# Kernel optimization log

Hardware: AMD Instinct MI355X
Metric: run time of the kernel (lower is better)

The kernel has to match this reference:

```python
import jax, jax.numpy as jnp
import numpy as np

B, H0, W0, C, NH, A, P = 32, 56, 56, 256, 8, 49, 7  # P = pool_size = sqrt(agent_num)
KS = 3  # depthwise conv kernel


def setup_inputs() -> dict:
    key = jax.random.key(0)
    ks = jax.random.split(key, 12)
    f32 = jnp.float32
    inp = {
        "x": jax.random.normal(ks[0], (B, H0 * W0, C), f32),
        "qkv_w": jax.random.normal(ks[1], (C, 3 * C), f32) * 0.02,   # used as x @ qkv_w
        "qkv_b": jax.random.normal(ks[2], (3 * C,), f32) * 0.02,
        "proj_w": jax.random.normal(ks[3], (C, C), f32) * 0.02,
        "proj_b": jax.random.normal(ks[4], (C,), f32) * 0.02,
        "dwc_w": jax.random.normal(ks[5], (C, 1, KS, KS), f32) * 0.1,  # depthwise OIHW, groups=C
        "dwc_b": jnp.zeros((C,), f32),
        "an_bias": jax.random.normal(ks[6], (NH, A, 7, 7), f32) * 0.02,
        "na_bias": jax.random.normal(ks[7], (NH, A, 7, 7), f32) * 0.02,
        "ah_bias": jax.random.normal(ks[8], (1, NH, A, H0, 1), f32) * 0.02,
        "aw_bias": jax.random.normal(ks[9], (1, NH, A, 1, W0), f32) * 0.02,
        "ha_bias": jax.random.normal(ks[10], (1, NH, H0, 1, A), f32) * 0.02,
        "wa_bias": jax.random.normal(ks[11], (1, NH, 1, W0, A), f32) * 0.02,
        "h": H0,
        "w": W0,
    }
    return inp


def _resize(t, hw):
    # bilinear (half-pixel, align_corners=False) resize of the last two dims
    return jax.image.resize(t, t.shape[:-2] + tuple(hw), method="bilinear")


def reference(x, qkv_w, qkv_b, proj_w, proj_b, dwc_w, dwc_b,
              an_bias, na_bias, ah_bias, aw_bias, ha_bias, wa_bias, h, w):
    b, n, c = x.shape
    nh = an_bias.shape[0]
    hd = c // nh
    a = an_bias.shape[1]
    p = int(a ** 0.5)
    scale = hd ** -0.5

    qkv = x @ qkv_w + qkv_b                      # (b, n, 3c)
    q, k, v = jnp.split(qkv, 3, axis=-1)

    # agent tokens: adaptive avg pool of q over (h, w) -> (p, p); exact since h%p==0
    q_img = q.reshape(b, h, w, c)
    agent = q_img.reshape(b, p, h // p, p, w // p, c).mean(axis=(2, 4)).reshape(b, a, c)

    q = q.reshape(b, n, nh, hd).transpose(0, 2, 1, 3)       # (b, nh, n, hd)
    k = k.reshape(b, n, nh, hd).transpose(0, 2, 1, 3)
    v = v.reshape(b, n, nh, hd).transpose(0, 2, 1, 3)
    agent = agent.reshape(b, a, nh, hd).transpose(0, 2, 1, 3)  # (b, nh, a, hd)

    def agent2token_bias(bias):  # (nh, a, h0, w0) -> (1, nh, a, n)
        pb = _resize(bias, (h, w)).reshape(nh, p, p, h * w).transpose(0, 3, 1, 2)
        pb = _resize(pb, (p, p)).reshape(nh, h * w, a).transpose(0, 2, 1)
        return pb[None]

    def token2agent_bias(bias):  # (nh, a, h0, w0) -> (1, nh, n, a)
        ab = _resize(bias, (h, w)).reshape(nh, p, p, h * w).transpose(0, 3, 1, 2)
        ab = _resize(ab, (p, p)).reshape(nh, h * w, a)
        return ab[None]

    position_bias = agent2token_bias(an_bias) + agent2token_bias((ah_bias + aw_bias)[0])
    agent_bias = token2agent_bias(na_bias) + \
        token2agent_bias((ha_bias + wa_bias)[0].transpose(0, 3, 1, 2))

    # stage 1: agent tokens attend to keys/values
    agent_attn = jax.nn.softmax(
        jnp.einsum('bhad,bhnd->bhan', agent * scale, k) + position_bias, axis=-1)
    agent_v = jnp.einsum('bhan,bhnd->bhad', agent_attn, v)      # (b, nh, a, hd)

    # stage 2: queries attend to agent tokens
    q_attn = jax.nn.softmax(
        jnp.einsum('bhnd,bhad->bhna', q * scale, agent) + agent_bias, axis=-1)
    out = jnp.einsum('bhna,bhad->bhnd', q_attn, agent_v)        # (b, nh, n, hd)
    out = out.transpose(0, 2, 1, 3).reshape(b, n, c)

    # depthwise conv on v
    v_img = v.transpose(0, 2, 1, 3).reshape(b, h, w, c).transpose(0, 3, 1, 2)  # NCHW
    dwc = jax.lax.conv_general_dilated(
        v_img, dwc_w, window_strides=(1, 1), padding='SAME',
        feature_group_count=c, dimension_numbers=('NCHW', 'OIHW', 'NCHW'))
    dwc = dwc + dwc_b[None, :, None, None]
    out = out + dwc.transpose(0, 2, 3, 1).reshape(b, n, c)

    return out @ proj_w + proj_b
```

## Files before the change

kernel.cpp:

```cpp
#include <hip/hip_runtime.h>
#include <stdint.h>

#define B_ 32
#define H_ 56
#define W_ 56
#define N_ 3136
#define C_ 256
#define NH_ 8
#define HD_ 32
#define A_ 49
#define NCH_ 7
#define CHK_ 448
#define SCALE_ 0.17677669529663687f

typedef _Float16 h16;
typedef __attribute__((ext_vector_type(4))) _Float16 h16x4;
typedef __attribute__((ext_vector_type(8))) _Float16 h16x8;
typedef __attribute__((ext_vector_type(4))) float f32x4;

__device__ __forceinline__ void gload16(const void* g, void* l) {
  __builtin_amdgcn_global_load_lds(
      (const __attribute__((address_space(1))) unsigned int*)(uintptr_t)g,
      (__attribute__((address_space(3))) unsigned int*)(unsigned int)(uintptr_t)l,
      16, 0, 0);
}

__global__ __launch_bounds__(256)
void bias_kernel(const float* __restrict__ an, const float* __restrict__ na,
                 const float* __restrict__ ah, const float* __restrict__ aw,
                 const float* __restrict__ ha, const float* __restrict__ wa,
                 float* __restrict__ posb, float* __restrict__ agbt)
{
  const int hh = blockIdx.x / A_;
  const int ag = blockIdx.x % A_;
  __shared__ float an7[A_], na7[A_], ahv[H_], awv[W_], hav[H_], wav[W_];
  const int tid = threadIdx.x;
  if (tid < A_) {
    an7[tid] = an[(hh*A_ + ag)*A_ + tid];
    na7[tid] = na[(hh*A_ + ag)*A_ + tid];
  }
  if (tid < H_) {
    ahv[tid] = ah[(hh*A_ + ag)*H_ + tid];
    awv[tid] = aw[(hh*A_ + ag)*W_ + tid];
    hav[tid] = ha[(hh*H_ + tid)*A_ + ag];
    wav[tid] = wa[(hh*W_ + tid)*A_ + ag];
  }
  __syncthreads();
  for (int t = tid; t < N_; t += 256) {
    const int ty = t / W_, tx = t % W_;
    const float py = (ty + 0.5f)*0.125f - 0.5f;
    const float px = (tx + 0.5f)*0.125f - 0.5f;
    const int iy = (int)floorf(py), ix = (int)floorf(px);
    const float fy = py - (float)iy, fx = px - (float)ix;
    const int iy0 = min(max(iy, 0), 6), iy1 = min(iy + 1, 6);
    const int ix0 = min(max(ix, 0), 6), ix1 = min(ix + 1, 6);
    const float w00 = (1.f-fy)*(1.f-fx), w01 = (1.f-fy)*fx;
    const float w10 = fy*(1.f-fx),       w11 = fy*fx;
    const float ban = w00*an7[iy0*7+ix0] + w01*an7[iy0*7+ix1]
                    + w10*an7[iy1*7+ix0] + w11*an7[iy1*7+ix1];
    const float bna = w00*na7[iy0*7+ix0] + w01*na7[iy0*7+ix1]
                    + w10*na7[iy1*7+ix0] + w11*na7[iy1*7+ix1];
    posb[((size_t)(hh*A_ + ag))*N_ + t] = ban + ahv[ty] + awv[tx];
    agbt[((size_t)(hh*A_ + ag))*N_ + t] = bna + hav[ty] + wav[tx];
  }
}

__global__ __launch_bounds__(256)
void convx_kernel(const float* __restrict__ x, h16* __restrict__ xh)
{
  const size_t nchunk = (size_t)B_*N_*C_/8;
  const size_t stride = (size_t)gridDim.x * 256;
  for (size_t i = blockIdx.x*256 + threadIdx.x; i < nchunk; i += stride) {
    const float4 u = ((const float4*)x)[i*2];
    const float4 v = ((const float4*)x)[i*2+1];
    h16x8 o;
    o[0]=(h16)u.x; o[1]=(h16)u.y; o[2]=(h16)u.z; o[3]=(h16)u.w;
    o[4]=(h16)v.x; o[5]=(h16)v.y; o[6]=(h16)v.z; o[7]=(h16)v.w;
    ((h16x8*)xh)[i] = o;
  }
}

__global__ __launch_bounds__(256)
void convw_kernel(const float* __restrict__ qkvw, const float* __restrict__ projw,
                  const float* __restrict__ dwcw, const float* __restrict__ dwcb,
                  h16* __restrict__ wtq, h16* __restrict__ wtp, h16* __restrict__ w9t)
{
  const int bid = blockIdx.x, k = threadIdx.x;
  if (bid < 768) {
    wtq[bid*256 + k] = (h16)qkvw[(size_t)k*768 + bid];
  } else if (bid < 1024) {
    const int n = bid - 768;
    wtp[n*256 + k] = (h16)projw[(size_t)k*256 + n];
  } else {
    const int row = bid - 1024;
    w9t[row*256 + k] = (h16)(row < 9 ? dwcw[k*9 + row] : dwcb[k]);
  }
}

__device__ __forceinline__ void gemm_tile_128(
    const h16* __restrict__ Ag, const h16* __restrict__ Bg,
    int m0, int n0, char* lds, f32x4 acc[4][4], int lane, int wr, int wc, int tid)
{
  int aoff[4], boff[4];
  #pragma unroll
  for (int r = 0; r < 4; ++r) {
    const int row = wr*64 + r*16 + (lane & 15);
    const int ps  = (lane >> 4) ^ ((row >> 1) & 3);
    aoff[r] = row*64 + ps*16;
  }
  #pragma unroll
  for (int c = 0; c < 4; ++c) {
    const int nrow = wc*64 + c*16 + (lane & 15);
    const int ps   = (lane >> 4) ^ ((nrow >> 1) & 3);
    boff[c] = 8192 + nrow*64 + ps*16;
  }
  const int i0 = tid, i1 = tid + 256;
  const int r0 = i0 >> 2, s0 = (i0 & 3) ^ ((r0 >> 1) & 3);
  const int r1 = i1 >> 2, s1 = (i1 & 3) ^ ((r1 >> 1) & 3);

  for (int k0 = 0; k0 < 256; k0 += 32) {
    __syncthreads();
    gload16(Ag + (size_t)(m0 + r0)*256 + k0 + s0*8, lds + i0*16);
    gload16(Ag + (size_t)(m0 + r1)*256 + k0 + s1*8, lds + i1*16);
    gload16(Bg + (size_t)(n0 + r0)*256 + k0 + s0*8, lds + 8192 + i0*16);
    gload16(Bg + (size_t)(n0 + r1)*256 + k0 + s1*8, lds + 8192 + i1*16);
    __syncthreads();
    h16x8 af[4], bf[4];
    #pragma unroll
    for (int r = 0; r < 4; ++r) af[r] = *(const h16x8*)(lds + aoff[r]);
    #pragma unroll
    for (int c = 0; c < 4; ++c) bf[c] = *(const h16x8*)(lds + boff[c]);
    #pragma unroll
    for (int r = 0; r < 4; ++r)
      #pragma unroll
      for (int c = 0; c < 4; ++c)
        acc[r][c] = __builtin_amdgcn_mfma_f32_16x16x32_f16(af[r], bf[c], acc[r][c], 0, 0, 0);
  }
}

__global__ __launch_bounds__(256)
void gemm_qkv_mfma(const h16* __restrict__ xh, const h16* __restrict__ wtq,
                   const float* __restrict__ qkvb,
                   h16* __restrict__ q, h16* __restrict__ k, h16* __restrict__ v)
{
  __shared__ __align__(16) char lds[16384];
  const int tid = threadIdx.x, lane = tid & 63, wid = tid >> 6;
  const int wr = wid & 1, wc = wid >> 1;
  const int m0 = blockIdx.y * 128, n0 = blockIdx.x * 128;
  f32x4 acc[4][4] = {};
  gemm_tile_128(xh, wtq, m0, n0, lds, acc, lane, wr, wc, tid);
  #pragma unroll
  for (int r = 0; r < 4; ++r) {
    #pragma unroll
    for (int reg = 0; reg < 4; ++reg) {
      const int m = m0 + wr*64 + r*16 + (lane >> 4)*4 + reg;
      const int bb = m / N_, t = m % N_;
      #pragma unroll
      for (int c = 0; c < 4; ++c) {
        const int n = n0 + wc*64 + c*16 + (lane & 15);
        const float val = acc[r][c][reg] + qkvb[n];
        const int part = n >> 8, cc = n & 255, hh = cc >> 5, d = cc & 31;
        h16* dst = (part == 0) ? q : ((part == 1) ? k : v);
        dst[(((size_t)(bb*NH_ + hh))*N_ + t)*HD_ + d] = (h16)val;
      }
    }
  }
}

__global__ __launch_bounds__(256)
void gemm_proj_mfma(const h16* __restrict__ preh, const h16* __restrict__ wtp,
                    const float* __restrict__ projb, float* __restrict__ out)
{
  __shared__ __align__(16) char lds[16384];
  const int tid = threadIdx.x, lane = tid & 63, wid = tid >> 6;
  const int wr = wid & 1, wc = wid >> 1;
  const int m0 = blockIdx.y * 128, n0 = blockIdx.x * 128;
  f32x4 acc[4][4] = {};
  gemm_tile_128(preh, wtp, m0, n0, lds, acc, lane, wr, wc, tid);
  #pragma unroll
  for (int r = 0; r < 4; ++r) {
    #pragma unroll
    for (int reg = 0; reg < 4; ++reg) {
      const int m = m0 + wr*64 + r*16 + (lane >> 4)*4 + reg;
      #pragma unroll
      for (int c = 0; c < 4; ++c) {
        const int n = n0 + wc*64 + c*16 + (lane & 15);
        out[(size_t)m*256 + n] = acc[r][c][reg] + projb[n];
      }
    }
  }
}

__global__ __launch_bounds__(64)
void pool_kernel(const h16* __restrict__ q, float* __restrict__ agent)
{
  const int blk = blockIdx.x;
  const int ag = blk % A_;
  const int rem = blk / A_;
  const int tid = threadIdx.x;
  const int d = tid & 31, half = tid >> 5;
  const int ay = ag / 7, ax = ag % 7;
  const size_t base = (size_t)rem * N_ * HD_;
  float s = 0.f;
  #pragma unroll
  for (int it = 0; it < 32; ++it) {
    const int yy = half*4 + (it >> 3), xx = it & 7;
    const int t = (ay*8 + yy)*W_ + ax*8 + xx;
    s += (float)q[base + (size_t)t*HD_ + d];
  }
  s += __shfl_down(s, 32, 64);
  if (tid < 32) agent[(size_t)rem*A_*HD_ + ag*HD_ + d] = s * (1.f/64.f);
}

__global__ __launch_bounds__(256)
void stage1a_mfma(const h16* __restrict__ kmat, const h16* __restrict__ vmat,
                  const float* __restrict__ agent, const float* __restrict__ posb,
                  float* __restrict__ pm, float* __restrict__ pl, float* __restrict__ pacc)
{
  __shared__ __align__(16) h16 Kl[64*32];
  __shared__ __align__(16) h16 Vt[32*72];
  __shared__ __align__(16) h16 Sl[64*72];
  const int tid = threadIdx.x, lane = tid & 63, wid = tid >> 6;
  const int bx = blockIdx.x;
  const int ch = bx % NCH_;
  const int rem = bx / NCH_;
  const int hh = rem & 7;
  const size_t kvbase = (size_t)rem * N_ * HD_;
  const size_t agbase = (size_t)rem * A_ * HD_;
  const float* pb = posb + (size_t)hh*A_*N_;

  const int arow = wid*16 + (lane & 15);
  const int kc = (lane >> 4) * 8;
  h16x8 a_ag = {};
  if (arow < A_) {
    #pragma unroll
    for (int j = 0; j < 8; ++j)
      a_ag[j] = (h16)(agent[agbase + (size_t)arow*HD_ + kc + j] * SCALE_);
  }

  const int r_k = tid >> 2;
  const int s_k = (tid & 3) ^ ((r_k >> 1) & 3);
  const int rowm = (lane >> 4) * 4;
  const int agrow0 = wid*16 + rowm;

  float m_r[4], l_r[4];
  #pragma unroll
  for (int r = 0; r < 4; ++r) { m_r[r] = -1e30f; l_r[r] = 0.f; }
  f32x4 accv[2] = {};

  for (int it = 0; it < 7; ++it) {
    const int t0 = ch*CHK_ + it*64;
    __syncthreads();
    gload16(kmat + kvbase + (size_t)(t0 + r_k)*HD_ + s_k*8, ((char*)Kl) + tid*16);
    const h16x8 vv = *(const h16x8*)&vmat[kvbase + (size_t)(t0 + lane)*HD_ + wid*8];
    #pragma unroll
    for (int j = 0; j < 8; ++j) Vt[(wid*8 + j)*72 + lane] = vv[j];
    __syncthreads();

    float sv[4][4];
    #pragma unroll
    for (int c = 0; c < 4; ++c) {
      const int kr = c*16 + (lane & 15);
      const int ph = (lane >> 4) ^ ((kr >> 1) & 3);
      const h16x8 bf = *(const h16x8*)&Kl[kr*32 + ph*8];
      const f32x4 sc = __builtin_amdgcn_mfma_f32_16x16x32_f16(a_ag, bf, (f32x4){0.f,0.f,0.f,0.f}, 0, 0, 0);
      #pragma unroll
      for (int reg = 0; reg < 4; ++reg) sv[reg][c] = sc[reg];
    }
    #pragma unroll
    for (int reg = 0; reg < 4; ++reg) {
      const int ag = agrow0 + reg;
      if (ag < A_) {
        #pragma unroll
        for (int c = 0; c < 4; ++c)
          sv[reg][c] += pb[(size_t)ag*N_ + t0 + c*16 + (lane & 15)];
      } else {
        #pragma unroll
        for (int c = 0; c < 4; ++c) sv[reg][c] = -1e30f;
      }
      float rm = fmaxf(fmaxf(sv[reg][0], sv[reg][1]), fmaxf(sv[reg][2], sv[reg][3]));
      rm = fmaxf(rm, __shfl_xor(rm, 1));
      rm = fmaxf(rm, __shfl_xor(rm, 2));
      rm = fmaxf(rm, __shfl_xor(rm, 4));
      rm = fmaxf(rm, __shfl_xor(rm, 8));
      const float mn = fmaxf(m_r[reg], rm);
      const float f = __expf(m_r[reg] - mn);
      m_r[reg] = mn;
      float rs = 0.f;
      #pragma unroll
      for (int c = 0; c < 4; ++c) {
        const float p = __expf(sv[reg][c] - mn);
        sv[reg][c] = p;
        rs += p;
      }
      rs += __shfl_xor(rs, 1); rs += __shfl_xor(rs, 2);
      rs += __shfl_xor(rs, 4); rs += __shfl_xor(rs, 8);
      l_r[reg] = l_r[reg]*f + rs;
      accv[0][reg] *= f;
      accv[1][reg] *= f;
      const int row = agrow0 + reg;
      #pragma unroll
      for (int c = 0; c < 4; ++c)
        Sl[row*72 + c*16 + (lane & 15)] = (h16)sv[reg][c];
    }
    __syncthreads();
    const int srow = wid*16 + (lane & 15);
    #pragma unroll
    for (int ks = 0; ks < 2; ++ks) {
      const h16x8 pf = *(const h16x8*)&Sl[srow*72 + ks*32 + (lane >> 4)*8];
      #pragma unroll
      for (int c2 = 0; c2 < 2; ++c2) {
        const int d = c2*16 + (lane & 15);
        const h16x8 vf = *(const h16x8*)&Vt[d*72 + ks*32 + (lane >> 4)*8];
        accv[c2] = __builtin_amdgcn_mfma_f32_16x16x32_f16(pf, vf, accv[c2], 0, 0, 0);
      }
    }
  }

  #pragma unroll
  for (int reg = 0; reg < 4; ++reg) {
    const int ag = agrow0 + reg;
    if (ag < A_) {
      if ((lane & 15) == 0) {
        pm[bx*A_ + ag] = m_r[reg];
        pl[bx*A_ + ag] = l_r[reg];
      }
      #pragma unroll
      for (int c2 = 0; c2 < 2; ++c2)
        pacc[(size_t)bx*(A_*HD_) + (size_t)ag*HD_ + c2*16 + (lane & 15)] = accv[c2][reg];
    }
  }
}

__global__ __launch_bounds__(256)
void stage1b_kernel(const float* __restrict__ pm, const float* __restrict__ pl,
                    const float* __restrict__ pacc, float* __restrict__ agv)
{
  const int rem = blockIdx.x;
  __shared__ float fs[NCH_*A_];
  const int tid = threadIdx.x;
  if (tid < A_) {
    float m = -1e30f;
    #pragma unroll
    for (int ch = 0; ch < NCH_; ++ch) m = fmaxf(m, pm[(rem*NCH_+ch)*A_ + tid]);
    float e[NCH_], l = 0.f;
    #pragma unroll
    for (int ch = 0; ch < NCH_; ++ch) {
      e[ch] = __expf(pm[(rem*NCH_+ch)*A_ + tid] - m);
      l += e[ch] * pl[(rem*NCH_+ch)*A_ + tid];
    }
    const float inv = 1.f / l;
    #pragma unroll
    for (int ch = 0; ch < NCH_; ++ch) fs[ch*A_ + tid] = e[ch] * inv;
  }
  __syncthreads();
  for (int idx = tid; idx < A_*HD_; idx += 256) {
    const int ag = idx >> 5;
    float s = 0.f;
    #pragma unroll
    for (int ch = 0; ch < NCH_; ++ch)
      s += fs[ch*A_ + ag] * pacc[((size_t)(rem*NCH_+ch))*(A_*HD_) + idx];
    agv[(size_t)rem*(A_*HD_) + idx] = s;
  }
}

__global__ __launch_bounds__(256)
void stage2_mfma(const h16* __restrict__ qmat, const float* __restrict__ agent,
                 const float* __restrict__ agv, const float* __restrict__ agbt,
                 h16* __restrict__ preh)
{
  __shared__ __align__(16) char lds2[45568];
  h16* Asw = (h16*)lds2;
  h16* AVt = (h16*)(lds2 + 4096);
  const int tid = threadIdx.x, lane = tid & 63, wid = tid >> 6;
  const int b = blockIdx.y >> 3, hh = blockIdx.y & 7;
  const size_t agbase = (size_t)(b*NH_ + hh)*A_*HD_;

  for (int i = tid; i < 64*32; i += 256) Asw[i] = (h16)0.f;
  for (int i = tid; i < 32*72; i += 256) AVt[i] = (h16)0.f;
  __syncthreads();
  for (int i = tid; i < A_*HD_; i += 256) {
    const int a = i >> 5, d = i & 31;
    Asw[a*32 + (((d >> 3) ^ ((a >> 1) & 3)))*8 + (d & 7)] = (h16)(agent[agbase + i] * SCALE_);
    AVt[d*72 + a] = (h16)agv[agbase + i];
  }
  __syncthreads();

  const int t0 = blockIdx.x*256 + wid*64;
  if (t0 >= N_) return;

  h16* Pl = (h16*)(lds2 + 8704 + wid*9216);
  const h16* qbase = qmat + (size_t)(b*NH_ + hh)*N_*HD_;
  const float* agbt_h = agbt + (size_t)hh*A_*N_;
  const int l15 = lane & 15, g = lane >> 4;

  h16x8 bq[4];
  #pragma unroll
  for (int c = 0; c < 4; ++c) {
    const int a = c*16 + l15;
    const int ph = g ^ ((a >> 1) & 3);
    bq[c] = *(const h16x8*)&Asw[a*32 + ph*8];
  }
  h16x8 aq[4];
  #pragma unroll
  for (int rt = 0; rt < 4; ++rt)
    aq[rt] = *(const h16x8*)&qbase[(size_t)(t0 + rt*16 + l15)*HD_ + g*8];

  f32x4 sc[4][4];
  #pragma unroll
  for (int rt = 0; rt < 4; ++rt)
    #pragma unroll
    for (int c = 0; c < 4; ++c)
      sc[rt][c] = __builtin_amdgcn_mfma_f32_16x16x32_f16(aq[rt], bq[c], (f32x4){0.f,0.f,0.f,0.f}, 0, 0, 0);

  #pragma unroll
  for (int rt = 0; rt < 4; ++rt) {
    float sv[4][4];
    #pragma unroll
    for (int c = 0; c < 4; ++c) {
      const int a = c*16 + l15;
      if (a < A_) {
        const float4 bias = *(const float4*)&agbt_h[(size_t)a*N_ + t0 + rt*16 + g*4];
        sv[0][c] = sc[rt][c][0] + bias.x;
        sv[1][c] = sc[rt][c][1] + bias.y;
        sv[2][c] = sc[rt][c][2] + bias.z;
        sv[3][c] = sc[rt][c][3] + bias.w;
      } else {
        sv[0][c] = sv[1][c] = sv[2][c] = sv[3][c] = -1e30f;
      }
    }
    #pragma unroll
    for (int reg = 0; reg < 4; ++reg) {
      float rm = fmaxf(fmaxf(sv[reg][0], sv[reg][1]), fmaxf(sv[reg][2], sv[reg][3]));
      rm = fmaxf(rm, __shfl_xor(rm, 1));
      rm = fmaxf(rm, __shfl_xor(rm, 2));
      rm = fmaxf(rm, __shfl_xor(rm, 4));
      rm = fmaxf(rm, __shfl_xor(rm, 8));
      float rs = 0.f;
      #pragma unroll
      for (int c = 0; c < 4; ++c) {
        const float p = __expf(sv[reg][c] - rm);
        sv[reg][c] = p;
        rs += p;
      }
      rs += __shfl_xor(rs, 1); rs += __shfl_xor(rs, 2);
      rs += __shfl_xor(rs, 4); rs += __shfl_xor(rs, 8);
      const float inv = 1.f / rs;
      const int row = rt*16 + g*4 + reg;
      #pragma unroll
      for (int c = 0; c < 4; ++c)
        Pl[row*72 + c*16 + l15] = (h16)(sv[reg][c] * inv);
    }
  }

  h16x8 vf[2][2];
  #pragma unroll
  for (int ks = 0; ks < 2; ++ks)
    #pragma unroll
    for (int c2 = 0; c2 < 2; ++c2)
      vf[ks][c2] = *(const h16x8*)&AVt[(c2*16 + l15)*72 + ks*32 + g*8];

  f32x4 av[4][2] = {};
  #pragma unroll
  for (int rt = 0; rt < 4; ++rt) {
    #pragma unroll
    for (int ks = 0; ks < 2; ++ks) {
      const h16x8 pf = *(const h16x8*)&Pl[(rt*16 + l15)*72 + ks*32 + g*8];
      #pragma unroll
      for (int c2 = 0; c2 < 2; ++c2)
        av[rt][c2] = __builtin_amdgcn_mfma_f32_16x16x32_f16(pf, vf[ks][c2], av[rt][c2], 0, 0, 0);
    }
  }

  #pragma unroll
  for (int rt = 0; rt < 4; ++rt)
    #pragma unroll
    for (int c2 = 0; c2 < 2; ++c2)
      #pragma unroll
      for (int reg = 0; reg < 4; ++reg) {
        const int t = t0 + rt*16 + g*4 + reg;
        preh[((size_t)b*N_ + t)*C_ + hh*HD_ + c2*16 + l15] = (h16)av[rt][c2][reg];
      }
}

__global__ __launch_bounds__(256)
void dwc_kernel(const h16* __restrict__ v, const h16* __restrict__ w9t,
                h16* __restrict__ preh)
{
  const int lin = blockIdx.x*256 + threadIdx.x;
  const int rem = blockIdx.y;
  const int t = lin >> 2, c8 = lin & 3;
  const int y = t / W_, x = t - y*W_;
  const int hh = rem & 7, b = rem >> 3;
  const int cbase = hh*HD_ + c8*8;

  h16x8 wk[9];
  #pragma unroll
  for (int k = 0; k < 9; ++k)
    wk[k] = *(const h16x8*)&w9t[k*C_ + cbase];
  h16x8 acc = *(const h16x8*)&w9t[9*C_ + cbase];

  const h16* vb = v + (size_t)rem*N_*HD_ + c8*8;
  #pragma unroll
  for (int ky = 0; ky < 3; ++ky) {
    #pragma unroll
    for (int kx = 0; kx < 3; ++kx) {
      const int yy = y + ky - 1, xx = x + kx - 1;
      const bool ok = ((unsigned)yy < (unsigned)H_) && ((unsigned)xx < (unsigned)W_);
      const int tt = ok ? (yy*W_ + xx) : t;
      const h16x8 vv = *(const h16x8*)&vb[(size_t)tt*HD_];
      const h16x8 w = ok ? wk[ky*3+kx] : (h16x8)(h16)0.f;
      acc += vv * w;
    }
  }

  h16x8* ph = (h16x8*)&preh[((size_t)b*N_ + t)*C_ + cbase];
  *ph += acc;
}

extern "C" void kernel_launch(void* const* d_in, const int* in_sizes, int n_in,
                              void* d_out, int out_size, void* d_ws, size_t ws_size,
                              hipStream_t stream)
{
  (void)in_sizes; (void)n_in; (void)out_size;
  const float* x     = (const float*)d_in[0];
  const float* qkvw  = (const float*)d_in[1];
  const float* qkvb  = (const float*)d_in[2];
  const float* projw = (const float*)d_in[3];
  const float* projb = (const float*)d_in[4];
  const float* dwcw  = (const float*)d_in[5];
  const float* dwcb  = (const float*)d_in[6];
  const float* an    = (const float*)d_in[7];
  const float* na    = (const float*)d_in[8];
  const float* ah    = (const float*)d_in[9];
  const float* aw    = (const float*)d_in[10];
  const float* ha    = (const float*)d_in[11];
  const float* wa    = (const float*)d_in[12];

  const size_t EL = (size_t)B_*N_*C_;
  char* ws = (char*)d_ws;
  h16*   qh    = (h16*)(ws);
  h16*   kh    = (h16*)(ws + EL*2);
  h16*   vh    = (h16*)(ws + EL*4);
  h16*   xh    = (h16*)(ws + EL*6);
  float* posb  = (float*)(ws + EL*8);
  float* agbt  = (float*)(ws + EL*8 + (size_t)NH_*A_*N_*4);
  float* agent = (float*)(ws + EL*8 + (size_t)NH_*A_*N_*8);
  float* agv   = (float*)(ws + EL*8 + (size_t)NH_*A_*N_*8 + (size_t)B_*NH_*A_*HD_*4);
  h16*   wtq   = (h16*)(ws + EL*8 + (size_t)NH_*A_*N_*8 + (size_t)B_*NH_*A_*HD_*8);
  h16*   wtp   = (h16*)((char*)wtq + (size_t)768*256*2);
  h16*   w9t   = (h16*)((char*)wtp + (size_t)256*256*2);
  const size_t NEED = EL*8 + (size_t)NH_*A_*N_*8 + (size_t)B_*NH_*A_*HD_*8
                    + (size_t)768*256*2 + (size_t)256*256*2 + (size_t)10*256*2;
  if (ws_size < NEED) return;

  float* pm   = (float*)xh;
  float* pl   = pm + (size_t)B_*NH_*NCH_*A_;
  float* pacc = pl + (size_t)B_*NH_*NCH_*A_;
  h16*   preh = kh;

  bias_kernel<<<dim3(NH_*A_), dim3(256), 0, stream>>>(an, na, ah, aw, ha, wa, posb, agbt);
  convx_kernel<<<dim3(4096), dim3(256), 0, stream>>>(x, xh);
  convw_kernel<<<dim3(1034), dim3(256), 0, stream>>>(qkvw, projw, dwcw, dwcb, wtq, wtp, w9t);
  gemm_qkv_mfma<<<dim3(6, 784), dim3(256), 0, stream>>>(xh, wtq, qkvb, qh, kh, vh);
  pool_kernel<<<dim3(B_*NH_*A_), dim3(64), 0, stream>>>(qh, agent);
  stage1a_mfma<<<dim3(B_*NH_*NCH_), dim3(256), 0, stream>>>(kh, vh, agent, posb, pm, pl, pacc);
  stage1b_kernel<<<dim3(B_*NH_), dim3(256), 0, stream>>>(pm, pl, pacc, agv);
  stage2_mfma<<<dim3(13, B_*NH_), dim3(256), 0, stream>>>(qh, agent, agv, agbt, preh);
  dwc_kernel<<<dim3(N_*4/256, B_*NH_), dim3(256), 0, stream>>>(vh, w9t, preh);
  gemm_proj_mfma<<<dim3(2, 784), dim3(256), 0, stream>>>(preh, wtp, projb, (float*)d_out);
}
```

Before: 332.3 us.

## Double-buffer GEMM LDS tiles and remap blocks for XCD-local L2 reuse

The shared GEMM tile loop now uses two LDS buffers. The next K-slice is issued with global_load_lds while MFMAs run on the current one, which drops one barrier per iteration. Both the QKV and projection GEMMs move to a 1D grid that assigns all N-tiles of an M-row tile to the same XCD, so the A rows should be reused in that XCD's L2. LDS use per block doubles to 32KB, which can lower occupancy. Correctness now relies on the async LDS loads having finished before the barrier.

After: 321.5 us. -3.2%, faster.

```diff
diff --git a/kernel.cpp b/kernel.cpp
--- a/kernel.cpp
+++ b/kernel.cpp
@@ -118,23 +118,33 @@
   const int r0 = i0 >> 2, s0 = (i0 & 3) ^ ((r0 >> 1) & 3);
   const int r1 = i1 >> 2, s1 = (i1 & 3) ^ ((r1 >> 1) & 3);
 
+  auto stage = [&](int buf, int k0) {
+    char* l = lds + buf*16384;
+    gload16(Ag + (size_t)(m0 + r0)*256 + k0 + s0*8, l + i0*16);
+    gload16(Ag + (size_t)(m0 + r1)*256 + k0 + s1*8, l + i1*16);
+    gload16(Bg + (size_t)(n0 + r0)*256 + k0 + s0*8, l + 8192 + i0*16);
+    gload16(Bg + (size_t)(n0 + r1)*256 + k0 + s1*8, l + 8192 + i1*16);
+  };
+
+  stage(0, 0);
+  __syncthreads();
+  int cur = 0;
+  #pragma unroll
   for (int k0 = 0; k0 < 256; k0 += 32) {
-    __syncthreads();
-    gload16(Ag + (size_t)(m0 + r0)*256 + k0 + s0*8, lds + i0*16);
-    gload16(Ag + (size_t)(m0 + r1)*256 + k0 + s1*8, lds + i1*16);
-    gload16(Bg + (size_t)(n0 + r0)*256 + k0 + s0*8, lds + 8192 + i0*16);
-    gload16(Bg + (size_t)(n0 + r1)*256 + k0 + s1*8, lds + 8192 + i1*16);
-    __syncthreads();
+    if (k0 + 32 < 256) stage(cur ^ 1, k0 + 32);
+    char* l = lds + cur*16384;
     h16x8 af[4], bf[4];
     #pragma unroll
-    for (int r = 0; r < 4; ++r) af[r] = *(const h16x8*)(lds + aoff[r]);
-    #pragma unroll
-    for (int c = 0; c < 4; ++c) bf[c] = *(const h16x8*)(lds + boff[c]);
+    for (int r = 0; r < 4; ++r) af[r] = *(const h16x8*)(l + aoff[r]);
+    #pragma unroll
+    for (int c = 0; c < 4; ++c) bf[c] = *(const h16x8*)(l + boff[c]);
     #pragma unroll
     for (int r = 0; r < 4; ++r)
       #pragma unroll
       for (int c = 0; c < 4; ++c)
         acc[r][c] = __builtin_amdgcn_mfma_f32_16x16x32_f16(af[r], bf[c], acc[r][c], 0, 0, 0);
+    __syncthreads();
+    cur ^= 1;
   }
 }
 
@@ -143,10 +153,13 @@
                    const float* __restrict__ qkvb,
                    h16* __restrict__ q, h16* __restrict__ k, h16* __restrict__ v)
 {
-  __shared__ __align__(16) char lds[16384];
+  __shared__ __align__(16) char lds[32768];
   const int tid = threadIdx.x, lane = tid & 63, wid = tid >> 6;
   const int wr = wid & 1, wc = wid >> 1;
-  const int m0 = blockIdx.y * 128, n0 = blockIdx.x * 128;
+  const int bid = blockIdx.x;
+  const int xcd = bid & 7, j = bid >> 3;
+  const int mt = xcd + 8*(j/6), nt = j - 6*(j/6);
+  const int m0 = mt*128, n0 = nt*128;
   f32x4 acc[4][4] = {};
   gemm_tile_128(xh, wtq, m0, n0, lds, acc, lane, wr, wc, tid);
   #pragma unroll
@@ -171,10 +184,13 @@
 void gemm_proj_mfma(const h16* __restrict__ preh, const h16* __restrict__ wtp,
                     const float* __restrict__ projb, float* __restrict__ out)
 {
-  __shared__ __align__(16) char lds[16384];
+  __shared__ __align__(16) char lds[32768];
   const int tid = threadIdx.x, lane = tid & 63, wid = tid >> 6;
   const int wr = wid & 1, wc = wid >> 1;
-  const int m0 = blockIdx.y * 128, n0 = blockIdx.x * 128;
+  const int bid = blockIdx.x;
+  const int xcd = bid & 7, j = bid >> 3;
+  const int mt = xcd + 8*(j >> 1), nt = j & 1;
+  const int m0 = mt*128, n0 = nt*128;
   f32x4 acc[4][4] = {};
   gemm_tile_128(preh, wtp, m0, n0, lds, acc, lane, wr, wc, tid);
   #pragma unroll
@@ -562,11 +578,11 @@
   bias_kernel<<<dim3(NH_*A_), dim3(256), 0, stream>>>(an, na, ah, aw, ha, wa, posb, agbt);
   convx_kernel<<<dim3(4096), dim3(256), 0, stream>>>(x, xh);
   convw_kernel<<<dim3(1034), dim3(256), 0, stream>>>(qkvw, projw, dwcw, dwcb, wtq, wtp, w9t);
-  gemm_qkv_mfma<<<dim3(6, 784), dim3(256), 0, stream>>>(xh, wtq, qkvb, qh, kh, vh);
+  gemm_qkv_mfma<<<dim3(4704), dim3(256), 0, stream>>>(xh, wtq, qkvb, qh, kh, vh);
   pool_kernel<<<dim3(B_*NH_*A_), dim3(64), 0, stream>>>(qh, agent);
   stage1a_mfma<<<dim3(B_*NH_*NCH_), dim3(256), 0, stream>>>(kh, vh, agent, posb, pm, pl, pacc);
   stage1b_kernel<<<dim3(B_*NH_), dim3(256), 0, stream>>>(pm, pl, pacc, agv);
   stage2_mfma<<<dim3(13, B_*NH_), dim3(256), 0, stream>>>(qh, agent, agv, agbt, preh);
   dwc_kernel<<<dim3(N_*4/256, B_*NH_), dim3(256), 0, stream>>>(vh, w9t, preh);
-  gemm_proj_mfma<<<dim3(2, 784), dim3(256), 0, stream>>>(preh, wtp, projb, (float*)d_out);
-}
+  gemm_proj_mfma<<<dim3(1568), dim3(256), 0, stream>>>(preh, wtp, projb, (float*)d_out);
+}
```
